# Performance work log

Hardware: AMD Instinct MI355X
Metric: run time of the kernel (lower is better)

## Reference

```python
import jax, jax.numpy as jnp
import numpy as np

N_NODES = 50000
N_EDGES = 800000
IN_CH = 128
OUT_CH = 64
BN_EPS = 1e-5


def setup_inputs() -> dict:
    key = jax.random.key(0)
    k1, k2, k3 = jax.random.split(key, 3)
    x = jax.random.normal(k1, (N_NODES, IN_CH), dtype=jnp.float32)
    edge_index = jax.random.randint(k2, (2, N_EDGES), 0, N_NODES, dtype=jnp.int64)
    W = jax.random.normal(k3, (IN_CH, OUT_CH), dtype=jnp.float32) / np.sqrt(IN_CH)
    bias = jnp.zeros((OUT_CH,), dtype=jnp.float32)
    gamma = jnp.ones((OUT_CH,), dtype=jnp.float32)
    beta = jnp.zeros((OUT_CH,), dtype=jnp.float32)
    return {"x": x, "edge_index": edge_index, "W": W, "bias": bias,
            "gamma": gamma, "beta": beta}


def reference(x, edge_index, W, bias, gamma, beta):
    N = x.shape[0]
    # Linear transform first (GCNConv order): [N, out]
    h = x @ W
    # Add self-loops
    loops = jnp.arange(N, dtype=edge_index.dtype)
    src = jnp.concatenate([edge_index[0], loops])  # [E+N]
    dst = jnp.concatenate([edge_index[1], loops])
    # Symmetric GCN normalization: deg^{-1/2}[src] * deg^{-1/2}[dst]
    ones = jnp.ones(dst.shape[0], dtype=h.dtype)
    deg = jax.ops.segment_sum(ones, dst, num_segments=N)
    dinv = jnp.where(deg > 0, jax.lax.rsqrt(deg), 0.0)
    norm = dinv[src] * dinv[dst]  # [E+N]
    # Gather, scale, scatter-add
    msgs = h[src] * norm[:, None]  # [E+N, out]
    agg = jax.ops.segment_sum(msgs, dst, num_segments=N) + bias  # [N, out]
    # tanh activation
    a = jnp.tanh(agg)
    # BatchNorm over node dim (training mode, biased var)
    mean = jnp.mean(a, axis=0)
    var = jnp.mean(jnp.square(a - mean), axis=0)
    return gamma * (a - mean) * jax.lax.rsqrt(var + BN_EPS) + beta
```

## Files before the change

### kernel.cpp

```cpp
#include <hip/hip_runtime.h>
#include <hip/hip_bf16.h>
#include <math.h>

#define N_NODES 50000
#define N_EDGES 800000
#define IN_CH 128
#define OUT_CH 64
#define BN_EPS 1e-5f
#define CAP 64

typedef __attribute__((ext_vector_type(8))) short short8;
typedef __attribute__((ext_vector_type(4))) float f32x4;

__device__ __forceinline__ float bf16u_to_f32(uint u) { return __uint_as_float(u << 16); }

__device__ __forceinline__ ushort f32_to_bf16(float f) {
    uint u = __float_as_uint(f);
    uint r = (u + 0x7fff + ((u >> 16) & 1)) >> 16;
    return (ushort)r;
}

__device__ __forceinline__ float fast_tanh(float x) {
    float xa = fminf(x, 30.0f);
    float e;
    asm("v_exp_f32 %0, %1" : "=v"(e) : "v"(xa * 2.8853900817779268f));
    float inv;
    asm("v_rcp_f32 %0, %1" : "=v"(inv) : "v"(e + 1.0f));
    return (e - 1.0f) * inv;
}

__global__ void fill_slots_kernel(const int4* __restrict__ esrc4, const int4* __restrict__ edst4,
                                  int* __restrict__ cnt, ushort* __restrict__ slot, int E4) {
    int i = blockIdx.x * blockDim.x + threadIdx.x;
    if (i < E4) {
        int4 s = esrc4[i];
        int4 d = edst4[i];
        int p;
        p = atomicAdd(&cnt[d.x], 1); if (p < CAP) slot[d.x * CAP + p] = (ushort)s.x;
        p = atomicAdd(&cnt[d.y], 1); if (p < CAP) slot[d.y * CAP + p] = (ushort)s.y;
        p = atomicAdd(&cnt[d.z], 1); if (p < CAP) slot[d.z * CAP + p] = (ushort)s.z;
        p = atomicAdd(&cnt[d.w], 1); if (p < CAP) slot[d.w * CAP + p] = (ushort)s.w;
    }
}

#define XPAD 136
__global__ __launch_bounds__(256) void gemm_mfma_kernel(const float* __restrict__ x,
                                                        const float* __restrict__ W,
                                                        const int* __restrict__ cnt,
                                                        ushort* __restrict__ hb, int N) {
    __shared__ ushort xs[64 * XPAD];
    __shared__ ushort wt[64 * XPAD];
    int t = threadIdx.x;
    int lane = t & 63;
    int w = t >> 6;
    int nn = lane & 15;
    int quad = lane >> 4;
    int row0 = blockIdx.x * 64;

#pragma unroll
    for (int i = 0; i < 32; ++i) {
        int wlin = t + 256 * i;
        int k = wlin >> 6, n = wlin & 63;
        wt[n * XPAD + k] = f32_to_bf16(W[wlin]);
    }
#pragma unroll
    for (int i = 0; i < 8; ++i) {
        int linear4 = t + 256 * i;
        int r = linear4 >> 5;
        int c4 = linear4 & 31;
        int gr = row0 + r; if (gr >= N) gr = N - 1;
        float4 v = *(const float4*)(x + (size_t)gr * IN_CH + c4 * 4);
        ushort u0 = f32_to_bf16(v.x), u1 = f32_to_bf16(v.y);
        ushort u2 = f32_to_bf16(v.z), u3 = f32_to_bf16(v.w);
        uint2 packed = make_uint2((uint)u0 | ((uint)u1 << 16), (uint)u2 | ((uint)u3 << 16));
        *(uint2*)&xs[r * XPAD + c4 * 4] = packed;
    }
    __syncthreads();

    short8 bfrag[4][4];
#pragma unroll
    for (int t2 = 0; t2 < 4; ++t2)
#pragma unroll
        for (int c = 0; c < 4; ++c)
            bfrag[t2][c] = *(const short8*)&wt[(16 * t2 + nn) * XPAD + 32 * c + quad * 8];

    f32x4 acc[4] = {{0.f, 0.f, 0.f, 0.f}, {0.f, 0.f, 0.f, 0.f},
                    {0.f, 0.f, 0.f, 0.f}, {0.f, 0.f, 0.f, 0.f}};
#pragma unroll
    for (int c = 0; c < 4; ++c) {
        short8 afrag = *(const short8*)&xs[(16 * w + nn) * XPAD + 32 * c + quad * 8];
#pragma unroll
        for (int t2 = 0; t2 < 4; ++t2)
            acc[t2] = __builtin_amdgcn_mfma_f32_16x16x32_bf16(afrag, bfrag[t2][c], acc[t2], 0, 0, 0);
    }

    int rbase = row0 + 16 * w + quad * 4;
    float dv[4];
#pragma unroll
    for (int r = 0; r < 4; ++r)
        dv[r] = (rbase + r < N) ? rsqrtf((float)(cnt[rbase + r] + 1)) : 0.f;
#pragma unroll
    for (int t2 = 0; t2 < 4; ++t2) {
#pragma unroll
        for (int r = 0; r < 4; ++r) {
            int row = rbase + r;
            if (row < N) hb[(size_t)row * OUT_CH + 16 * t2 + nn] = f32_to_bf16(acc[t2][r] * dv[r]);
        }
    }
}

__global__ __launch_bounds__(256) void gather_fused_kernel(const int* __restrict__ cnt,
                                                           const ushort* __restrict__ slot,
                                                           const ushort* __restrict__ hb,
                                                           const float* __restrict__ bias,
                                                           float* __restrict__ out,
                                                           float* __restrict__ sums, int N) {
    int t = threadIdx.x;
    int lane = t & 63;
    int g = lane >> 3;
    int sub = lane & 7;
    int cidx = 8 * sub + (((g & 1) << 2) | (g & 2) | ((g >> 2) & 1));
    int wid = (blockIdx.x * blockDim.x + t) >> 6;
    int nw = (gridDim.x * blockDim.x) >> 6;
    float bias_c = bias[cidx];
    float ssum = 0.f, ssq = 0.f;

#define ISSUE(J, H0, H1) do {                                              \
        int e0 = (J) + g, e1 = e0 + 8;                                     \
        int i0 = e0 - 1; i0 = (i0 < 0) ? 0 : i0;                           \
        int s0 = __shfl(sv, i0);                                           \
        int s1 = __shfl(sv, e1 - 1);                                       \
        s0 = (e0 == 0) ? d : s0;                                           \
        s0 = (e0 < M) ? s0 : N_NODES;                                      \
        s1 = (e1 < M) ? s1 : N_NODES;                                      \
        H0 = *(const uint4*)(hb + ((size_t)s0 << 6) + (sub << 3));         \
        H1 = *(const uint4*)(hb + ((size_t)s1 << 6) + (sub << 3));         \
    } while (0)

#define CONSUME(H)                                                          \
        a0 += __uint_as_float((H).x << 16); a1 += __uint_as_float((H).x & 0xffff0000u); \
        a2 += __uint_as_float((H).y << 16); a3 += __uint_as_float((H).y & 0xffff0000u); \
        a4 += __uint_as_float((H).z << 16); a5 += __uint_as_float((H).z & 0xffff0000u); \
        a6 += __uint_as_float((H).w << 16); a7 += __uint_as_float((H).w & 0xffff0000u);

    int d = wid;
    int m_n = 0, sv_n = 0;
    if (d < N) {
        m_n = cnt[d];
        sv_n = __builtin_nontemporal_load(&slot[(size_t)d * CAP + lane]);
    }

    while (d < N) {
        int mraw = m_n;
        int sv = sv_n;
        float dd = rsqrtf((float)(mraw + 1));
        int m = mraw; if (m > CAP) m = CAP;
        int M = m + 1;

        int dn = d + nw;
        if (dn < N) {
            m_n = cnt[dn];
            sv_n = __builtin_nontemporal_load(&slot[(size_t)dn * CAP + lane]);
        }

        float a0 = 0.f, a1 = 0.f, a2 = 0.f, a3 = 0.f;
        float a4 = 0.f, a5 = 0.f, a6 = 0.f, a7 = 0.f;

        uint4 h0, h1;
        ISSUE(0, h0, h1);
        for (int j = 16; j < M; j += 16) {
            uint4 n0, n1;
            ISSUE(j, n0, n1);
            CONSUME(h0); CONSUME(h1);
            h0 = n0; h1 = n1;
        }
        CONSUME(h0); CONSUME(h1);

        float b0, b1, b2, b3;
        {
            float s0 = a0 + __shfl_xor(a0, 8);
            float s1 = a1 + __shfl_xor(a1, 8);
            float s2 = a2 + __shfl_xor(a2, 8);
            float s3 = a3 + __shfl_xor(a3, 8);
            float s4 = a4 + __shfl_xor(a4, 8);
            float s5 = a5 + __shfl_xor(a5, 8);
            float s6 = a6 + __shfl_xor(a6, 8);
            float s7 = a7 + __shfl_xor(a7, 8);
            bool hi = (g & 1);
            b0 = hi ? s4 : s0; b1 = hi ? s5 : s1; b2 = hi ? s6 : s2; b3 = hi ? s7 : s3;
        }
        float c0, c1;
        {
            float s0 = b0 + __shfl_xor(b0, 16);
            float s1 = b1 + __shfl_xor(b1, 16);
            float s2 = b2 + __shfl_xor(b2, 16);
            float s3 = b3 + __shfl_xor(b3, 16);
            bool hi = (g & 2);
            c0 = hi ? s2 : s0; c1 = hi ? s3 : s1;
        }
        float total;
        {
            float s0 = c0 + __shfl_xor(c0, 32);
            float s1 = c1 + __shfl_xor(c1, 32);
            total = (g & 4) ? s1 : s0;
        }

        float v = fast_tanh(fmaf(dd, total, bias_c));
        out[(size_t)d * OUT_CH + cidx] = v;
        ssum += v;
        ssq += v * v;

        d = dn;
    }
#undef ISSUE
#undef CONSUME

    __shared__ float ls[256];
    __shared__ float ls2[256];
    ls[t] = ssum; ls2[t] = ssq;
    __syncthreads();
    if (t < 128) { ls[t] += ls[t + 128]; ls2[t] += ls2[t + 128]; }
    __syncthreads();
    if (t < 64) {
        atomicAdd(&sums[cidx], ls[t] + ls[t + 64]);
        atomicAdd(&sums[64 + cidx], ls2[t] + ls2[t + 64]);
    }
}

__global__ __launch_bounds__(256) void bn_apply_kernel(float4* __restrict__ a,
                                                       const float* __restrict__ sums,
                                                       const float* __restrict__ gamma,
                                                       const float* __restrict__ beta, int total4) {
    int c0 = (threadIdx.x * 4) & 63;
    const float invN = 1.0f / (float)N_NODES;
    float4 scale, shift;
    {
        float m0 = sums[c0 + 0] * invN, m1 = sums[c0 + 1] * invN;
        float m2 = sums[c0 + 2] * invN, m3 = sums[c0 + 3] * invN;
        float v0 = sums[64 + c0 + 0] * invN - m0 * m0;
        float v1 = sums[64 + c0 + 1] * invN - m1 * m1;
        float v2 = sums[64 + c0 + 2] * invN - m2 * m2;
        float v3 = sums[64 + c0 + 3] * invN - m3 * m3;
        scale.x = gamma[c0 + 0] * rsqrtf(v0 + BN_EPS);
        scale.y = gamma[c0 + 1] * rsqrtf(v1 + BN_EPS);
        scale.z = gamma[c0 + 2] * rsqrtf(v2 + BN_EPS);
        scale.w = gamma[c0 + 3] * rsqrtf(v3 + BN_EPS);
        shift.x = beta[c0 + 0] - m0 * scale.x;
        shift.y = beta[c0 + 1] - m1 * scale.y;
        shift.z = beta[c0 + 2] - m2 * scale.z;
        shift.w = beta[c0 + 3] - m3 * scale.w;
    }
    int stride = gridDim.x * blockDim.x;
    for (int idx = blockIdx.x * blockDim.x + threadIdx.x; idx < total4; idx += stride) {
        float4 v = a[idx];
        v.x = v.x * scale.x + shift.x;
        v.y = v.y * scale.y + shift.y;
        v.z = v.z * scale.z + shift.z;
        v.w = v.w * scale.w + shift.w;
        a[idx] = v;
    }
}

extern "C" void kernel_launch(void* const* d_in, const int* in_sizes, int n_in,
                              void* d_out, int out_size, void* d_ws, size_t ws_size,
                              hipStream_t stream) {
    const float* x     = (const float*)d_in[0];
    const int*   eidx  = (const int*)d_in[1];
    const float* W     = (const float*)d_in[2];
    const float* bias  = (const float*)d_in[3];
    const float* gamma = (const float*)d_in[4];
    const float* beta  = (const float*)d_in[5];
    float* out = (float*)d_out;

    const int4* esrc4 = (const int4*)eidx;
    const int4* edst4 = (const int4*)(eidx + N_EDGES);

    ushort* slot = (ushort*)d_ws;
    int*   cnt   = (int*)(slot + (size_t)N_NODES * CAP);
    float* sums  = (float*)(cnt + N_NODES);
    ushort* hb   = (ushort*)(sums + 128);

    size_t zero_span = (size_t)N_NODES * 4 + 128 * 4 + (size_t)(N_NODES + 1) * OUT_CH * 2;
    hipMemsetAsync(cnt, 0, zero_span, stream);
    fill_slots_kernel<<<(N_EDGES / 4 + 255) / 256, 256, 0, stream>>>(esrc4, edst4, cnt, slot, N_EDGES / 4);
    gemm_mfma_kernel<<<(N_NODES + 63) / 64, 256, 0, stream>>>(x, W, cnt, hb, N_NODES);
    gather_fused_kernel<<<2048, 256, 0, stream>>>(cnt, slot, hb, bias, out, sums, N_NODES);
    bn_apply_kernel<<<512, 256, 0, stream>>>((float4*)out, sums, gamma, beta, N_NODES * OUT_CH / 4);
}
```

Before: 208.2 us.

## Reorder workspace to shrink memset, scalarize edge fill, vectorize W load

The workspace is reordered so that only the zero sentinel row of hb, the degree counts and the BN sums are cleared, instead of the whole hb buffer. The edge-fill kernel now handles one edge per thread instead of four, which exposes more parallelism for the atomics. The GEMM loads W as float4 while transposing it into shared memory. The gather kernel drops its software prefetch of the next node's count and slot row in favour of a simple strided loop, which may leave that load latency exposed.

```diff
diff --git a/kernel.cpp b/kernel.cpp
--- a/kernel.cpp
+++ b/kernel.cpp
@@ -29,17 +29,14 @@
     return (e - 1.0f) * inv;
 }
 
-__global__ void fill_slots_kernel(const int4* __restrict__ esrc4, const int4* __restrict__ edst4,
-                                  int* __restrict__ cnt, ushort* __restrict__ slot, int E4) {
+__global__ void fill_slots_kernel(const int* __restrict__ esrc, const int* __restrict__ edst,
+                                  int* __restrict__ cnt, ushort* __restrict__ slot, int E) {
     int i = blockIdx.x * blockDim.x + threadIdx.x;
-    if (i < E4) {
-        int4 s = esrc4[i];
-        int4 d = edst4[i];
-        int p;
-        p = atomicAdd(&cnt[d.x], 1); if (p < CAP) slot[d.x * CAP + p] = (ushort)s.x;
-        p = atomicAdd(&cnt[d.y], 1); if (p < CAP) slot[d.y * CAP + p] = (ushort)s.y;
-        p = atomicAdd(&cnt[d.z], 1); if (p < CAP) slot[d.z * CAP + p] = (ushort)s.z;
-        p = atomicAdd(&cnt[d.w], 1); if (p < CAP) slot[d.w * CAP + p] = (ushort)s.w;
+    if (i < E) {
+        int s = esrc[i];
+        int d = edst[i];
+        int p = atomicAdd(&cnt[d], 1);
+        if (p < CAP) slot[d * CAP + p] = (ushort)s;
     }
 }
 
@@ -57,11 +54,18 @@
     int quad = lane >> 4;
     int row0 = blockIdx.x * 64;
 
-#pragma unroll
-    for (int i = 0; i < 32; ++i) {
-        int wlin = t + 256 * i;
-        int k = wlin >> 6, n = wlin & 63;
-        wt[n * XPAD + k] = f32_to_bf16(W[wlin]);
+    const float4* W4 = (const float4*)W;
+#pragma unroll
+    for (int i = 0; i < 8; ++i) {
+        int f4 = t + 256 * i;
+        float4 v = W4[f4];
+        int e0 = f4 * 4;
+        int k = e0 >> 6;
+        int n = e0 & 63;
+        wt[(n + 0) * XPAD + k] = f32_to_bf16(v.x);
+        wt[(n + 1) * XPAD + k] = f32_to_bf16(v.y);
+        wt[(n + 2) * XPAD + k] = f32_to_bf16(v.z);
+        wt[(n + 3) * XPAD + k] = f32_to_bf16(v.w);
     }
 #pragma unroll
     for (int i = 0; i < 8; ++i) {
@@ -143,25 +147,12 @@
         a4 += __uint_as_float((H).z << 16); a5 += __uint_as_float((H).z & 0xffff0000u); \
         a6 += __uint_as_float((H).w << 16); a7 += __uint_as_float((H).w & 0xffff0000u);
 
-    int d = wid;
-    int m_n = 0, sv_n = 0;
-    if (d < N) {
-        m_n = cnt[d];
-        sv_n = __builtin_nontemporal_load(&slot[(size_t)d * CAP + lane]);
-    }
-
-    while (d < N) {
-        int mraw = m_n;
-        int sv = sv_n;
+    for (int d = wid; d < N; d += nw) {
+        int mraw = cnt[d];
         float dd = rsqrtf((float)(mraw + 1));
         int m = mraw; if (m > CAP) m = CAP;
         int M = m + 1;
-
-        int dn = d + nw;
-        if (dn < N) {
-            m_n = cnt[dn];
-            sv_n = __builtin_nontemporal_load(&slot[(size_t)dn * CAP + lane]);
-        }
+        int sv = __builtin_nontemporal_load(&slot[(size_t)d * CAP + lane]);
 
         float a0 = 0.f, a1 = 0.f, a2 = 0.f, a3 = 0.f;
         float a4 = 0.f, a5 = 0.f, a6 = 0.f, a7 = 0.f;
@@ -209,8 +200,6 @@
         out[(size_t)d * OUT_CH + cidx] = v;
         ssum += v;
         ssq += v * v;
-
-        d = dn;
     }
 #undef ISSUE
 #undef CONSUME
@@ -272,17 +261,17 @@
     const float* beta  = (const float*)d_in[5];
     float* out = (float*)d_out;
 
-    const int4* esrc4 = (const int4*)eidx;
-    const int4* edst4 = (const int4*)(eidx + N_EDGES);
-
-    ushort* slot = (ushort*)d_ws;
-    int*   cnt   = (int*)(slot + (size_t)N_NODES * CAP);
+    const int* esrc = eidx;
+    const int* edst = eidx + N_EDGES;
+
+    ushort* hb   = (ushort*)d_ws;
+    int*   cnt   = (int*)(hb + (size_t)(N_NODES + 1) * OUT_CH);
     float* sums  = (float*)(cnt + N_NODES);
-    ushort* hb   = (ushort*)(sums + 128);
-
-    size_t zero_span = (size_t)N_NODES * 4 + 128 * 4 + (size_t)(N_NODES + 1) * OUT_CH * 2;
-    hipMemsetAsync(cnt, 0, zero_span, stream);
-    fill_slots_kernel<<<(N_EDGES / 4 + 255) / 256, 256, 0, stream>>>(esrc4, edst4, cnt, slot, N_EDGES / 4);
+    ushort* slot = (ushort*)(((uintptr_t)(sums + 128) + 255) & ~(uintptr_t)255);
+
+    size_t zero_span = (size_t)OUT_CH * 2 + (size_t)N_NODES * 4 + 128 * 4;
+    hipMemsetAsync(hb + (size_t)N_NODES * OUT_CH, 0, zero_span, stream);
+    fill_slots_kernel<<<(N_EDGES + 255) / 256, 256, 0, stream>>>(esrc, edst, cnt, slot, N_EDGES);
     gemm_mfma_kernel<<<(N_NODES + 63) / 64, 256, 0, stream>>>(x, W, cnt, hb, N_NODES);
     gather_fused_kernel<<<2048, 256, 0, stream>>>(cnt, slot, hb, bias, out, sums, N_NODES);
     bn_apply_kernel<<<512, 256, 0, stream>>>((float4*)out, sums, gamma, beta, N_NODES * OUT_CH / 4);
```

Result: faster. 202.2 us (-2.9%).
